# Kernel optimization log

Measured on AMD Instinct MI355X. Metric: run time of the kernel, lower is better.

The kernel has to match this reference:

```python
import jax, jax.numpy as jnp
import numpy as np

THRESHOLD = 1.5
MIN_AREA = 3
B, H, W = 8, 1024, 1024


def _label_components(mask):
    """8-connectivity connected-component labeling by min-index propagation.
    mask: [B,H,W] bool. Returns int32 labels [B,H,W]; each component is labeled
    by the minimum global flat index of its pixels; background pixels = B*H*W.
    Labels are globally unique across the batch (matches sort_labels' per-batch
    unique relabeling up to a label permutation).
    """
    N = B * H * W
    SENT = jnp.int32(N)
    flat = jnp.arange(N, dtype=jnp.int32).reshape(B, H, W)
    lab0 = jnp.where(mask, flat, SENT)

    def neighbor_min(lab):
        p = jnp.pad(lab, ((0, 0), (1, 1), (1, 1)), constant_values=N)
        m = lab
        for dr in (-1, 0, 1):
            for dc in (-1, 0, 1):
                if dr == 0 and dc == 0:
                    continue
                m = jnp.minimum(m, p[:, 1 + dr:1 + dr + H, 1 + dc:1 + dc + W])
        return jnp.where(mask, m, SENT)

    def cond(state):
        return state[1]

    def body(state):
        lab, _ = state
        new = neighbor_min(lab)
        return new, jnp.any(new != lab)

    lab, _ = jax.lax.while_loop(cond, body, (lab0, jnp.array(True)))
    return lab


def setup_inputs() -> dict:
    key = jax.random.key(0)
    x = jax.random.normal(key, (B, H, W // 1), dtype=jnp.float32)
    return {"input_tensor": x.reshape(B, 1, H, W)}


def reference(input_tensor):
    """Dense encoding of the original ragged output: for every pixel belonging
    to a cluster with area > MIN_AREA, emit the cluster's max value and the
    (row, col) of the first (lowest flat index) occurrence of that max;
    background / small-cluster pixels get (0, -1, -1). Since THRESHOLD > 0,
    max over masked_fill(0) in the original equals max over cluster pixels.
    """
    x = input_tensor[:, 0]                  # [B,H,W]
    N = B * H * W
    nseg = N + 1                            # last segment = background
    mask = (x >= THRESHOLD)
    ids = _label_components(mask).reshape(-1)          # [N] int32 in [0, N]
    vals = x.reshape(-1)
    fg = mask.reshape(-1)

    area = jax.ops.segment_sum(fg.astype(jnp.float32), ids, num_segments=nseg)
    cmax = jax.ops.segment_max(vals, ids, num_segments=nseg)

    within = jnp.tile(jnp.arange(H * W, dtype=jnp.int32), B)  # flat idx in image
    is_max = (vals == cmax[ids]) & fg
    cand = jnp.where(is_max, within, jnp.int32(H * W))
    amin = jax.ops.segment_min(cand, ids, num_segments=nseg)  # first argmax

    valid = fg & (area[ids] > MIN_AREA)
    out_max = jnp.where(valid, cmax[ids], jnp.float32(0.0)).reshape(B, H, W)
    aidx = amin[ids]
    row = jnp.where(valid, aidx // W, jnp.int32(-1)).reshape(B, H, W)
    col = jnp.where(valid, aidx % W, jnp.int32(-1)).reshape(B, H, W)
    return out_max, row, col
```

## Files before the change

### kernel.cpp

```cpp
#include <hip/hip_runtime.h>
#include <stdint.h>

#define THRESH 1.5f
constexpr int NPIX = 8 * 1024 * 1024;
constexpr int HW   = 1024 * 1024;
constexpr int WW   = 1024;
constexpr int NWORD = NPIX / 32;
constexpr int WPR   = WW / 32;

constexpr int BLK     = 256;
constexpr int GRD_PX4 = NPIX / (BLK * 4);
constexpr int GRD_W   = NWORD / BLK;

constexpr int SPB        = 640;
constexpr int BASE_SLOTS = GRD_W * SPB;
constexpr int OVF_SLOTS  = 16384;
constexpr int CAP        = BASE_SLOTS + OVF_SLOTS;

constexpr int WLSTRIDE = 1024;

__device__ __forceinline__ int find_root(const int* __restrict__ P, int x) {
    int p = P[x];
    while (p != x && p < NPIX) { x = p; p = P[x]; }
    return x;
}

__device__ __forceinline__ void merge(int* P, int a, int b) {
    int ra = find_root(P, a);
    int rb = find_root(P, b);
    while (ra != rb) {
        if (ra < rb) { int t = ra; ra = rb; rb = t; }
        int old = atomicCAS(&P[ra], ra, rb);
        if (old == ra) break;
        ra = find_root(P, old);
        rb = find_root(P, rb);
    }
}

__global__ void mask_init_k(const float* __restrict__ x, int* __restrict__ parent,
                            unsigned* __restrict__ mask, uint2* __restrict__ wl,
                            int* __restrict__ wl_cnt, int* __restrict__ ovf) {
    __shared__ unsigned s_nib[BLK];
    __shared__ int s_rank;
    int t  = threadIdx.x;
    int gt = blockIdx.x * BLK + t;
    int i4 = gt * 4;
    float4 v = *(const float4*)(x + i4);
    unsigned nib = (unsigned)(v.x >= THRESH) | ((unsigned)(v.y >= THRESH) << 1) |
                   ((unsigned)(v.z >= THRESH) << 2) | ((unsigned)(v.w >= THRESH) << 3);
    *(int4*)(parent + i4) = make_int4(i4, i4 + 1, i4 + 2, i4 + 3);
    if (t == 0) s_rank = 0;
    s_nib[t] = nib;
    __syncthreads();
    if ((t & 7) == 0) {
        unsigned w = 0;
        #pragma unroll
        for (int k = 0; k < 8; k++) w |= s_nib[t + k] << (4 * k);
        mask[gt >> 3] = w;
    }
    int nfg = __popc(nib);
    if (nfg) {
        int r = atomicAdd(&s_rank, nfg);
        uint2* dst = wl + (size_t)blockIdx.x * WLSTRIDE;
        if (nib & 1u) dst[r++] = make_uint2((unsigned)i4,     __float_as_uint(v.x));
        if (nib & 2u) dst[r++] = make_uint2((unsigned)i4 + 1, __float_as_uint(v.y));
        if (nib & 4u) dst[r++] = make_uint2((unsigned)i4 + 2, __float_as_uint(v.z));
        if (nib & 8u) dst[r++] = make_uint2((unsigned)i4 + 3, __float_as_uint(v.w));
    }
    __syncthreads();
    if (t == 0) wl_cnt[blockIdx.x] = s_rank;
    if (gt == 0) *ovf = 0;
}

__global__ void union_k(const unsigned* __restrict__ mask, int* __restrict__ parent) {
    int w = blockIdx.x * BLK + threadIdx.x;
    unsigned cur = mask[w];
    if (!cur) return;
    int r  = (w >> 5) & (WW - 1);
    int cw = w & (WPR - 1);
    unsigned prev = (cw > 0) ? mask[w - 1] : 0u;
    unsigned above = 0u, abovePrev = 0u, aboveNext = 0u;
    if (r > 0) {
        above     = mask[w - WPR];
        abovePrev = (cw > 0)       ? mask[w - WPR - 1] : 0u;
        aboveNext = (cw < WPR - 1) ? mask[w - WPR + 1] : 0u;
    }
    int base = w << 5;
    unsigned mW  = cur & ((cur   << 1) | (prev      >> 31));
    unsigned mN  = cur & above;
    unsigned mNW = cur & ((above << 1) | (abovePrev >> 31));
    unsigned mNE = cur & ((above >> 1) | ((aboveNext & 1u) << 31));
    while (mW)  { int b = __ffs(mW)  - 1; mW  &= mW  - 1; merge(parent, base + b, base + b - 1); }
    while (mN)  { int b = __ffs(mN)  - 1; mN  &= mN  - 1; merge(parent, base + b, base + b - WW); }
    while (mNW) { int b = __ffs(mNW) - 1; mNW &= mNW - 1; merge(parent, base + b, base + b - WW - 1); }
    while (mNE) { int b = __ffs(mNE) - 1; mNE &= mNE - 1; merge(parent, base + b, base + b - WW + 1); }
}

__global__ void claim_k(const unsigned* __restrict__ mask, int* __restrict__ parent,
                        int* __restrict__ cnt, unsigned long long* __restrict__ best,
                        int* __restrict__ ovf) {
    __shared__ int s_cnt;
    if (threadIdx.x == 0) s_cnt = 0;
    __syncthreads();
    int w = blockIdx.x * BLK + threadIdx.x;
    unsigned cur = mask[w];
    int base = w << 5;
    while (cur) {
        int b = __ffs(cur) - 1; cur &= cur - 1;
        int p = base + b;
        int root = find_root(parent, p);
        if (root == p) {
            int rank = atomicAdd(&s_cnt, 1);
            int slot;
            if (rank < SPB) slot = blockIdx.x * SPB + rank;
            else { int o = atomicAdd(ovf, 1); slot = BASE_SLOTS + (o < OVF_SLOTS ? o : OVF_SLOTS - 1); }
            cnt[slot] = 0; best[slot] = 0ull;
            parent[p] = NPIX + slot;
        } else {
            parent[p] = root;
        }
    }
}

__device__ __forceinline__ int compact_id(const int* __restrict__ P, int p) {
    int e = P[p];
    if (e < NPIX) e = P[e];
    return e - NPIX;
}

__global__ void stats_k(const uint2* __restrict__ wl, const int* __restrict__ wl_cnt,
                        const int* __restrict__ parent, int* __restrict__ cnt,
                        unsigned long long* __restrict__ best) {
    int region = blockIdx.x;
    int c = wl_cnt[region];
    const uint2* src = wl + (size_t)region * WLSTRIDE;
    for (int j = threadIdx.x; j < c; j += 64) {
        uint2 e = src[j];
        int p = (int)e.x;
        int cid = compact_id(parent, p);
        if (cid < 0 || cid >= CAP) continue;
        atomicAdd(&cnt[cid], 1);
        unsigned within = (unsigned)(p & (HW - 1));
        unsigned long long pk =
            ((unsigned long long)e.y << 32) | (unsigned long long)(~within);
        atomicMax(&best[cid], pk);
    }
}

__device__ __forceinline__ void lookup_one(const int* __restrict__ parent,
                                           const int* __restrict__ cnt,
                                           const unsigned long long* __restrict__ best,
                                           int p, float& om, float& orow, float& ocol) {
    int cid = compact_id(parent, p);
    if (cid >= 0 && cid < CAP && cnt[cid] > 3) {
        unsigned long long pk = best[cid];
        om   = __uint_as_float((unsigned)(pk >> 32));
        unsigned idx = ~((unsigned)pk);
        orow = (float)(idx >> 10);
        ocol = (float)(idx & (WW - 1));
    }
}

__global__ void out_k(const unsigned* __restrict__ mask, const int* __restrict__ parent,
                      const int* __restrict__ cnt,
                      const unsigned long long* __restrict__ best,
                      float* __restrict__ o) {
    int t = blockIdx.x * BLK + threadIdx.x;
    unsigned nib = (mask[t >> 3] >> ((t & 7) * 4)) & 0xFu;
    int i4 = t * 4;
    float4 m  = make_float4(0.f, 0.f, 0.f, 0.f);
    float4 rr = make_float4(-1.f, -1.f, -1.f, -1.f);
    float4 cc = make_float4(-1.f, -1.f, -1.f, -1.f);
    if (nib) {
        if (nib & 1u) lookup_one(parent, cnt, best, i4,     m.x, rr.x, cc.x);
        if (nib & 2u) lookup_one(parent, cnt, best, i4 + 1, m.y, rr.y, cc.y);
        if (nib & 4u) lookup_one(parent, cnt, best, i4 + 2, m.z, rr.z, cc.z);
        if (nib & 8u) lookup_one(parent, cnt, best, i4 + 3, m.w, rr.w, cc.w);
    }
    *(float4*)(o + i4)            = m;
    *(float4*)(o + NPIX + i4)     = rr;
    *(float4*)(o + 2 * NPIX + i4) = cc;
}

extern "C" void kernel_launch(void* const* d_in, const int* in_sizes, int n_in,
                              void* d_out, int out_size, void* d_ws, size_t ws_size,
                              hipStream_t stream) {
    const float* x = (const float*)d_in[0];
    float* o = (float*)d_out;

    char* base = (char*)d_ws;
    int* parent = (int*)base;
    size_t off = (size_t)NPIX * 4;
    unsigned long long* best = (unsigned long long*)(base + off);  off += (size_t)CAP * 8;
    int* cnt       = (int*)(base + off);                           off += (size_t)CAP * 4;
    unsigned* mask = (unsigned*)(base + off);                      off += (size_t)NWORD * 4;
    int* wl_cnt    = (int*)(base + off);                           off += (size_t)GRD_PX4 * 4;
    uint2* wl      = (uint2*)(base + off);                         off += (size_t)GRD_PX4 * WLSTRIDE * 8;
    int* ovf       = (int*)(base + off);

    mask_init_k<<<GRD_PX4, BLK, 0, stream>>>(x, parent, mask, wl, wl_cnt, ovf);
    union_k    <<<GRD_W,   BLK, 0, stream>>>(mask, parent);
    claim_k    <<<GRD_W,   BLK, 0, stream>>>(mask, parent, cnt, best, ovf);
    stats_k    <<<GRD_PX4, 64,  0, stream>>>(wl, wl_cnt, parent, cnt, best);
    out_k      <<<GRD_PX4, BLK, 0, stream>>>(mask, parent, cnt, best, o);
}
```

Before: 203.3 us.

## Fuse five CCL kernels into one cooperative kernel with grid syncs

Replaces the five separate launches (mask/init, union, claim, stats, output) with a single cooperative kernel of 1024 blocks that steps through the same phases, separated by grid-wide syncs. Phases 1 and 5 loop over several regions per block, and the stats phase assigns one wavefront per region. This is meant to remove launch gaps and per-kernel tail effects. In exchange it requires all blocks to be co-resident, limits occupancy to a fixed grid, and pays for grid.sync barriers.

```diff
diff --git a/kernel.cpp b/kernel.cpp
--- a/kernel.cpp
+++ b/kernel.cpp
@@ -1,19 +1,24 @@
 #include <hip/hip_runtime.h>
+#include <hip/hip_cooperative_groups.h>
 #include <stdint.h>
 
+namespace cg = cooperative_groups;
+
 #define THRESH 1.5f
-constexpr int NPIX = 8 * 1024 * 1024;
-constexpr int HW   = 1024 * 1024;
-constexpr int WW   = 1024;
+constexpr int NPIX  = 8 * 1024 * 1024;
+constexpr int HW    = 1024 * 1024;
+constexpr int WW    = 1024;
 constexpr int NWORD = NPIX / 32;
 constexpr int WPR   = WW / 32;
 
-constexpr int BLK     = 256;
-constexpr int GRD_PX4 = NPIX / (BLK * 4);
-constexpr int GRD_W   = NWORD / BLK;
+constexpr int BLK   = 256;
+constexpr int GRID  = 1024;
+constexpr int REGIONS  = NPIX / (BLK * 4);
+constexpr int P1_ITERS = REGIONS / GRID;
+static_assert(GRID * BLK == NWORD, "phase 2/3 assume exactly 1 word per thread");
 
 constexpr int SPB        = 640;
-constexpr int BASE_SLOTS = GRD_W * SPB;
+constexpr int BASE_SLOTS = GRID * SPB;
 constexpr int OVF_SLOTS  = 16384;
 constexpr int CAP        = BASE_SLOTS + OVF_SLOTS;
 
@@ -37,114 +42,10 @@
     }
 }
 
-__global__ void mask_init_k(const float* __restrict__ x, int* __restrict__ parent,
-                            unsigned* __restrict__ mask, uint2* __restrict__ wl,
-                            int* __restrict__ wl_cnt, int* __restrict__ ovf) {
-    __shared__ unsigned s_nib[BLK];
-    __shared__ int s_rank;
-    int t  = threadIdx.x;
-    int gt = blockIdx.x * BLK + t;
-    int i4 = gt * 4;
-    float4 v = *(const float4*)(x + i4);
-    unsigned nib = (unsigned)(v.x >= THRESH) | ((unsigned)(v.y >= THRESH) << 1) |
-                   ((unsigned)(v.z >= THRESH) << 2) | ((unsigned)(v.w >= THRESH) << 3);
-    *(int4*)(parent + i4) = make_int4(i4, i4 + 1, i4 + 2, i4 + 3);
-    if (t == 0) s_rank = 0;
-    s_nib[t] = nib;
-    __syncthreads();
-    if ((t & 7) == 0) {
-        unsigned w = 0;
-        #pragma unroll
-        for (int k = 0; k < 8; k++) w |= s_nib[t + k] << (4 * k);
-        mask[gt >> 3] = w;
-    }
-    int nfg = __popc(nib);
-    if (nfg) {
-        int r = atomicAdd(&s_rank, nfg);
-        uint2* dst = wl + (size_t)blockIdx.x * WLSTRIDE;
-        if (nib & 1u) dst[r++] = make_uint2((unsigned)i4,     __float_as_uint(v.x));
-        if (nib & 2u) dst[r++] = make_uint2((unsigned)i4 + 1, __float_as_uint(v.y));
-        if (nib & 4u) dst[r++] = make_uint2((unsigned)i4 + 2, __float_as_uint(v.z));
-        if (nib & 8u) dst[r++] = make_uint2((unsigned)i4 + 3, __float_as_uint(v.w));
-    }
-    __syncthreads();
-    if (t == 0) wl_cnt[blockIdx.x] = s_rank;
-    if (gt == 0) *ovf = 0;
-}
-
-__global__ void union_k(const unsigned* __restrict__ mask, int* __restrict__ parent) {
-    int w = blockIdx.x * BLK + threadIdx.x;
-    unsigned cur = mask[w];
-    if (!cur) return;
-    int r  = (w >> 5) & (WW - 1);
-    int cw = w & (WPR - 1);
-    unsigned prev = (cw > 0) ? mask[w - 1] : 0u;
-    unsigned above = 0u, abovePrev = 0u, aboveNext = 0u;
-    if (r > 0) {
-        above     = mask[w - WPR];
-        abovePrev = (cw > 0)       ? mask[w - WPR - 1] : 0u;
-        aboveNext = (cw < WPR - 1) ? mask[w - WPR + 1] : 0u;
-    }
-    int base = w << 5;
-    unsigned mW  = cur & ((cur   << 1) | (prev      >> 31));
-    unsigned mN  = cur & above;
-    unsigned mNW = cur & ((above << 1) | (abovePrev >> 31));
-    unsigned mNE = cur & ((above >> 1) | ((aboveNext & 1u) << 31));
-    while (mW)  { int b = __ffs(mW)  - 1; mW  &= mW  - 1; merge(parent, base + b, base + b - 1); }
-    while (mN)  { int b = __ffs(mN)  - 1; mN  &= mN  - 1; merge(parent, base + b, base + b - WW); }
-    while (mNW) { int b = __ffs(mNW) - 1; mNW &= mNW - 1; merge(parent, base + b, base + b - WW - 1); }
-    while (mNE) { int b = __ffs(mNE) - 1; mNE &= mNE - 1; merge(parent, base + b, base + b - WW + 1); }
-}
-
-__global__ void claim_k(const unsigned* __restrict__ mask, int* __restrict__ parent,
-                        int* __restrict__ cnt, unsigned long long* __restrict__ best,
-                        int* __restrict__ ovf) {
-    __shared__ int s_cnt;
-    if (threadIdx.x == 0) s_cnt = 0;
-    __syncthreads();
-    int w = blockIdx.x * BLK + threadIdx.x;
-    unsigned cur = mask[w];
-    int base = w << 5;
-    while (cur) {
-        int b = __ffs(cur) - 1; cur &= cur - 1;
-        int p = base + b;
-        int root = find_root(parent, p);
-        if (root == p) {
-            int rank = atomicAdd(&s_cnt, 1);
-            int slot;
-            if (rank < SPB) slot = blockIdx.x * SPB + rank;
-            else { int o = atomicAdd(ovf, 1); slot = BASE_SLOTS + (o < OVF_SLOTS ? o : OVF_SLOTS - 1); }
-            cnt[slot] = 0; best[slot] = 0ull;
-            parent[p] = NPIX + slot;
-        } else {
-            parent[p] = root;
-        }
-    }
-}
-
 __device__ __forceinline__ int compact_id(const int* __restrict__ P, int p) {
     int e = P[p];
     if (e < NPIX) e = P[e];
     return e - NPIX;
-}
-
-__global__ void stats_k(const uint2* __restrict__ wl, const int* __restrict__ wl_cnt,
-                        const int* __restrict__ parent, int* __restrict__ cnt,
-                        unsigned long long* __restrict__ best) {
-    int region = blockIdx.x;
-    int c = wl_cnt[region];
-    const uint2* src = wl + (size_t)region * WLSTRIDE;
-    for (int j = threadIdx.x; j < c; j += 64) {
-        uint2 e = src[j];
-        int p = (int)e.x;
-        int cid = compact_id(parent, p);
-        if (cid < 0 || cid >= CAP) continue;
-        atomicAdd(&cnt[cid], 1);
-        unsigned within = (unsigned)(p & (HW - 1));
-        unsigned long long pk =
-            ((unsigned long long)e.y << 32) | (unsigned long long)(~within);
-        atomicMax(&best[cid], pk);
-    }
 }
 
 __device__ __forceinline__ void lookup_one(const int* __restrict__ parent,
@@ -161,25 +62,140 @@
     }
 }
 
-__global__ void out_k(const unsigned* __restrict__ mask, const int* __restrict__ parent,
-                      const int* __restrict__ cnt,
-                      const unsigned long long* __restrict__ best,
-                      float* __restrict__ o) {
-    int t = blockIdx.x * BLK + threadIdx.x;
-    unsigned nib = (mask[t >> 3] >> ((t & 7) * 4)) & 0xFu;
-    int i4 = t * 4;
-    float4 m  = make_float4(0.f, 0.f, 0.f, 0.f);
-    float4 rr = make_float4(-1.f, -1.f, -1.f, -1.f);
-    float4 cc = make_float4(-1.f, -1.f, -1.f, -1.f);
-    if (nib) {
-        if (nib & 1u) lookup_one(parent, cnt, best, i4,     m.x, rr.x, cc.x);
-        if (nib & 2u) lookup_one(parent, cnt, best, i4 + 1, m.y, rr.y, cc.y);
-        if (nib & 4u) lookup_one(parent, cnt, best, i4 + 2, m.z, rr.z, cc.z);
-        if (nib & 8u) lookup_one(parent, cnt, best, i4 + 3, m.w, rr.w, cc.w);
-    }
-    *(float4*)(o + i4)            = m;
-    *(float4*)(o + NPIX + i4)     = rr;
-    *(float4*)(o + 2 * NPIX + i4) = cc;
+__global__ __launch_bounds__(BLK, 4) void fused_k(
+    const float* __restrict__ x, float* __restrict__ o,
+    int* __restrict__ parent, unsigned* __restrict__ mask,
+    uint2* __restrict__ wl, int* __restrict__ wl_cnt,
+    int* __restrict__ cnt, unsigned long long* __restrict__ best,
+    int* __restrict__ ovf)
+{
+    cg::grid_group grid = cg::this_grid();
+    __shared__ unsigned s_nib[BLK];
+    __shared__ int s_rank;
+    __shared__ int s_cnt;
+    const int t = threadIdx.x;
+
+    if (blockIdx.x == 0 && t == 0) *ovf = 0;
+
+    for (int it = 0; it < P1_ITERS; ++it) {
+        int v  = (int)blockIdx.x + it * GRID;
+        int gt = v * BLK + t;
+        int i4 = gt * 4;
+        float4 vx = *(const float4*)(x + i4);
+        unsigned nib = (unsigned)(vx.x >= THRESH) | ((unsigned)(vx.y >= THRESH) << 1) |
+                       ((unsigned)(vx.z >= THRESH) << 2) | ((unsigned)(vx.w >= THRESH) << 3);
+        *(int4*)(parent + i4) = make_int4(i4, i4 + 1, i4 + 2, i4 + 3);
+        if (t == 0) s_rank = 0;
+        s_nib[t] = nib;
+        __syncthreads();
+        if ((t & 7) == 0) {
+            unsigned w = 0;
+            #pragma unroll
+            for (int k = 0; k < 8; k++) w |= s_nib[t + k] << (4 * k);
+            mask[gt >> 3] = w;
+        }
+        int nfg = __popc(nib);
+        if (nfg) {
+            int r = atomicAdd(&s_rank, nfg);
+            uint2* dst = wl + (size_t)v * WLSTRIDE;
+            if (nib & 1u) dst[r++] = make_uint2((unsigned)i4,     __float_as_uint(vx.x));
+            if (nib & 2u) dst[r++] = make_uint2((unsigned)i4 + 1, __float_as_uint(vx.y));
+            if (nib & 4u) dst[r++] = make_uint2((unsigned)i4 + 2, __float_as_uint(vx.z));
+            if (nib & 8u) dst[r++] = make_uint2((unsigned)i4 + 3, __float_as_uint(vx.w));
+        }
+        __syncthreads();
+        if (t == 0) wl_cnt[v] = s_rank;
+    }
+    grid.sync();
+
+    {
+        int w = blockIdx.x * BLK + t;
+        unsigned cur = mask[w];
+        if (cur) {
+            int r  = (w >> 5) & (WW - 1);
+            int cw = w & (WPR - 1);
+            unsigned prev = (cw > 0) ? mask[w - 1] : 0u;
+            unsigned above = 0u, abovePrev = 0u, aboveNext = 0u;
+            if (r > 0) {
+                above     = mask[w - WPR];
+                abovePrev = (cw > 0)       ? mask[w - WPR - 1] : 0u;
+                aboveNext = (cw < WPR - 1) ? mask[w - WPR + 1] : 0u;
+            }
+            int base = w << 5;
+            unsigned mW  = cur & ((cur   << 1) | (prev      >> 31));
+            unsigned mN  = cur & above;
+            unsigned mNW = cur & ((above << 1) | (abovePrev >> 31));
+            unsigned mNE = cur & ((above >> 1) | ((aboveNext & 1u) << 31));
+            while (mW)  { int b = __ffs(mW)  - 1; mW  &= mW  - 1; merge(parent, base + b, base + b - 1); }
+            while (mN)  { int b = __ffs(mN)  - 1; mN  &= mN  - 1; merge(parent, base + b, base + b - WW); }
+            while (mNW) { int b = __ffs(mNW) - 1; mNW &= mNW - 1; merge(parent, base + b, base + b - WW - 1); }
+            while (mNE) { int b = __ffs(mNE) - 1; mNE &= mNE - 1; merge(parent, base + b, base + b - WW + 1); }
+        }
+    }
+    grid.sync();
+
+    {
+        if (t == 0) s_cnt = 0;
+        __syncthreads();
+        int w = blockIdx.x * BLK + t;
+        unsigned cur = mask[w];
+        int base = w << 5;
+        while (cur) {
+            int b = __ffs(cur) - 1; cur &= cur - 1;
+            int p = base + b;
+            int root = find_root(parent, p);
+            if (root == p) {
+                int rank = atomicAdd(&s_cnt, 1);
+                int slot;
+                if (rank < SPB) slot = blockIdx.x * SPB + rank;
+                else { int ofo = atomicAdd(ovf, 1); slot = BASE_SLOTS + (ofo < OVF_SLOTS ? ofo : OVF_SLOTS - 1); }
+                cnt[slot] = 0; best[slot] = 0ull;
+                parent[p] = NPIX + slot;
+            } else {
+                parent[p] = root;
+            }
+        }
+    }
+    grid.sync();
+
+    {
+        int gw   = (int)blockIdx.x * (BLK / 64) + (t >> 6);
+        int lane = t & 63;
+        for (int r = gw; r < REGIONS; r += GRID * (BLK / 64)) {
+            int c = wl_cnt[r];
+            const uint2* src = wl + (size_t)r * WLSTRIDE;
+            for (int j = lane; j < c; j += 64) {
+                uint2 e = src[j];
+                int p = (int)e.x;
+                int cid = compact_id(parent, p);
+                if (cid < 0 || cid >= CAP) continue;
+                atomicAdd(&cnt[cid], 1);
+                unsigned within = (unsigned)(p & (HW - 1));
+                unsigned long long pk =
+                    ((unsigned long long)e.y << 32) | (unsigned long long)(~within);
+                atomicMax(&best[cid], pk);
+            }
+        }
+    }
+    grid.sync();
+
+    for (int it = 0; it < P1_ITERS; ++it) {
+        int tt = ((int)blockIdx.x + it * GRID) * BLK + t;
+        unsigned nib = (mask[tt >> 3] >> ((tt & 7) * 4)) & 0xFu;
+        int i4 = tt * 4;
+        float4 m  = make_float4(0.f, 0.f, 0.f, 0.f);
+        float4 rr = make_float4(-1.f, -1.f, -1.f, -1.f);
+        float4 cc = make_float4(-1.f, -1.f, -1.f, -1.f);
+        if (nib) {
+            if (nib & 1u) lookup_one(parent, cnt, best, i4,     m.x, rr.x, cc.x);
+            if (nib & 2u) lookup_one(parent, cnt, best, i4 + 1, m.y, rr.y, cc.y);
+            if (nib & 4u) lookup_one(parent, cnt, best, i4 + 2, m.z, rr.z, cc.z);
+            if (nib & 8u) lookup_one(parent, cnt, best, i4 + 3, m.w, rr.w, cc.w);
+        }
+        *(float4*)(o + i4)            = m;
+        *(float4*)(o + NPIX + i4)     = rr;
+        *(float4*)(o + 2 * NPIX + i4) = cc;
+    }
 }
 
 extern "C" void kernel_launch(void* const* d_in, const int* in_sizes, int n_in,
@@ -194,13 +210,13 @@
     unsigned long long* best = (unsigned long long*)(base + off);  off += (size_t)CAP * 8;
     int* cnt       = (int*)(base + off);                           off += (size_t)CAP * 4;
     unsigned* mask = (unsigned*)(base + off);                      off += (size_t)NWORD * 4;
-    int* wl_cnt    = (int*)(base + off);                           off += (size_t)GRD_PX4 * 4;
-    uint2* wl      = (uint2*)(base + off);                         off += (size_t)GRD_PX4 * WLSTRIDE * 8;
+    int* wl_cnt    = (int*)(base + off);                           off += (size_t)REGIONS * 4;
+    uint2* wl      = (uint2*)(base + off);                         off += (size_t)REGIONS * WLSTRIDE * 8;
     int* ovf       = (int*)(base + off);
 
-    mask_init_k<<<GRD_PX4, BLK, 0, stream>>>(x, parent, mask, wl, wl_cnt, ovf);
-    union_k    <<<GRD_W,   BLK, 0, stream>>>(mask, parent);
-    claim_k    <<<GRD_W,   BLK, 0, stream>>>(mask, parent, cnt, best, ovf);
-    stats_k    <<<GRD_PX4, 64,  0, stream>>>(wl, wl_cnt, parent, cnt, best);
-    out_k      <<<GRD_PX4, BLK, 0, stream>>>(mask, parent, cnt, best, o);
-}
+    void* args[] = { (void*)&x, (void*)&o, (void*)&parent, (void*)&mask,
+                     (void*)&wl, (void*)&wl_cnt, (void*)&cnt, (void*)&best,
+                     (void*)&ovf };
+    hipLaunchCooperativeKernel((const void*)fused_k, dim3(GRID), dim3(BLK),
+                               args, 0, stream);
+}
```

Result: slower. 702.0 us (+245.2%).

## Fuse root claiming into stats kernel with lazy CAS-based compact ids

Applied to the files above, without the earlier changes.

Drops the separate claim kernel, which walked every mask word and path-compressed every pixel. Roots are now claimed lazily inside the stats pass: a global atomic counter hands out slots and a CAS marks each root, and each pixel's parent is overwritten with its compact id. The cnt and best tables are zeroed up front in mask_init, so the output lookup becomes a single parent read. The cost is contention on one global counter and racing CAS claims, with some slots wasted when a CAS loses, plus the extra zeroing writes.

```diff
diff --git a/kernel.cpp b/kernel.cpp
--- a/kernel.cpp
+++ b/kernel.cpp
@@ -2,9 +2,9 @@
 #include <stdint.h>
 
 #define THRESH 1.5f
-constexpr int NPIX = 8 * 1024 * 1024;
-constexpr int HW   = 1024 * 1024;
-constexpr int WW   = 1024;
+constexpr int NPIX  = 8 * 1024 * 1024;
+constexpr int HW    = 1024 * 1024;
+constexpr int WW    = 1024;
 constexpr int NWORD = NPIX / 32;
 constexpr int WPR   = WW / 32;
 
@@ -12,10 +12,9 @@
 constexpr int GRD_PX4 = NPIX / (BLK * 4);
 constexpr int GRD_W   = NWORD / BLK;
 
-constexpr int SPB        = 640;
-constexpr int BASE_SLOTS = GRD_W * SPB;
-constexpr int OVF_SLOTS  = 16384;
-constexpr int CAP        = BASE_SLOTS + OVF_SLOTS;
+constexpr int CAP = 671744;
+constexpr int ZINT4 = CAP * 12 / 16;
+static_assert((CAP * 12) % 16 == 0, "zero region must be int4-divisible");
 
 constexpr int WLSTRIDE = 1024;
 
@@ -39,11 +38,13 @@
 
 __global__ void mask_init_k(const float* __restrict__ x, int* __restrict__ parent,
                             unsigned* __restrict__ mask, uint2* __restrict__ wl,
-                            int* __restrict__ wl_cnt, int* __restrict__ ovf) {
+                            int* __restrict__ wl_cnt, int4* __restrict__ zbase,
+                            int* __restrict__ gcnt) {
     __shared__ unsigned s_nib[BLK];
     __shared__ int s_rank;
     int t  = threadIdx.x;
     int gt = blockIdx.x * BLK + t;
+    if (gt < ZINT4) zbase[gt] = make_int4(0, 0, 0, 0);
     int i4 = gt * 4;
     float4 v = *(const float4*)(x + i4);
     unsigned nib = (unsigned)(v.x >= THRESH) | ((unsigned)(v.y >= THRESH) << 1) |
@@ -69,7 +70,7 @@
     }
     __syncthreads();
     if (t == 0) wl_cnt[blockIdx.x] = s_rank;
-    if (gt == 0) *ovf = 0;
+    if (gt == 0) *gcnt = 0;
 }
 
 __global__ void union_k(const unsigned* __restrict__ mask, int* __restrict__ parent) {
@@ -96,49 +97,38 @@
     while (mNE) { int b = __ffs(mNE) - 1; mNE &= mNE - 1; merge(parent, base + b, base + b - WW + 1); }
 }
 
-__global__ void claim_k(const unsigned* __restrict__ mask, int* __restrict__ parent,
-                        int* __restrict__ cnt, unsigned long long* __restrict__ best,
-                        int* __restrict__ ovf) {
-    __shared__ int s_cnt;
-    if (threadIdx.x == 0) s_cnt = 0;
-    __syncthreads();
-    int w = blockIdx.x * BLK + threadIdx.x;
-    unsigned cur = mask[w];
-    int base = w << 5;
-    while (cur) {
-        int b = __ffs(cur) - 1; cur &= cur - 1;
-        int p = base + b;
-        int root = find_root(parent, p);
-        if (root == p) {
-            int rank = atomicAdd(&s_cnt, 1);
-            int slot;
-            if (rank < SPB) slot = blockIdx.x * SPB + rank;
-            else { int o = atomicAdd(ovf, 1); slot = BASE_SLOTS + (o < OVF_SLOTS ? o : OVF_SLOTS - 1); }
-            cnt[slot] = 0; best[slot] = 0ull;
-            parent[p] = NPIX + slot;
+__device__ __forceinline__ int claim_cid(int* __restrict__ P, int p,
+                                         int* __restrict__ gcnt) {
+    int x = p;
+    while (true) {
+        int e = P[x];
+        if (e >= NPIX) return e - NPIX;
+        if (e == x) {
+            int slot = atomicAdd(gcnt, 1);
+            if (slot >= CAP) slot = CAP - 1;
+            int old = atomicCAS(&P[x], x, NPIX + slot);
+            if (old == x)     return slot;
+            if (old >= NPIX)  return old - NPIX;
+            x = old;
         } else {
-            parent[p] = root;
+            x = e;
         }
     }
 }
 
-__device__ __forceinline__ int compact_id(const int* __restrict__ P, int p) {
-    int e = P[p];
-    if (e < NPIX) e = P[e];
-    return e - NPIX;
-}
-
-__global__ void stats_k(const uint2* __restrict__ wl, const int* __restrict__ wl_cnt,
-                        const int* __restrict__ parent, int* __restrict__ cnt,
-                        unsigned long long* __restrict__ best) {
+__global__ void cstats_k(const uint2* __restrict__ wl, const int* __restrict__ wl_cnt,
+                         int* __restrict__ parent, int* __restrict__ cnt,
+                         unsigned long long* __restrict__ best,
+                         int* __restrict__ gcnt) {
     int region = blockIdx.x;
     int c = wl_cnt[region];
     const uint2* src = wl + (size_t)region * WLSTRIDE;
     for (int j = threadIdx.x; j < c; j += 64) {
         uint2 e = src[j];
         int p = (int)e.x;
-        int cid = compact_id(parent, p);
+        int cid = claim_cid(parent, p, gcnt);
         if (cid < 0 || cid >= CAP) continue;
+        parent[p] = NPIX + cid;
         atomicAdd(&cnt[cid], 1);
         unsigned within = (unsigned)(p & (HW - 1));
         unsigned long long pk =
@@ -151,7 +141,7 @@
                                            const int* __restrict__ cnt,
                                            const unsigned long long* __restrict__ best,
                                            int p, float& om, float& orow, float& ocol) {
-    int cid = compact_id(parent, p);
+    int cid = parent[p] - NPIX;
     if (cid >= 0 && cid < CAP && cnt[cid] > 3) {
         unsigned long long pk = best[cid];
         om   = __uint_as_float((unsigned)(pk >> 32));
@@ -191,16 +181,16 @@
     char* base = (char*)d_ws;
     int* parent = (int*)base;
     size_t off = (size_t)NPIX * 4;
-    unsigned long long* best = (unsigned long long*)(base + off);  off += (size_t)CAP * 8;
+    unsigned long long* best = (unsigned long long*)(base + off);
+    int4* zbase = (int4*)(base + off);                             off += (size_t)CAP * 8;
     int* cnt       = (int*)(base + off);                           off += (size_t)CAP * 4;
     unsigned* mask = (unsigned*)(base + off);                      off += (size_t)NWORD * 4;
     int* wl_cnt    = (int*)(base + off);                           off += (size_t)GRD_PX4 * 4;
     uint2* wl      = (uint2*)(base + off);                         off += (size_t)GRD_PX4 * WLSTRIDE * 8;
-    int* ovf       = (int*)(base + off);
+    int* gcnt      = (int*)(base + off);
 
-    mask_init_k<<<GRD_PX4, BLK, 0, stream>>>(x, parent, mask, wl, wl_cnt, ovf);
+    mask_init_k<<<GRD_PX4, BLK, 0, stream>>>(x, parent, mask, wl, wl_cnt, zbase, gcnt);
     union_k    <<<GRD_W,   BLK, 0, stream>>>(mask, parent);
-    claim_k    <<<GRD_W,   BLK, 0, stream>>>(mask, parent, cnt, best, ovf);
-    stats_k    <<<GRD_PX4, 64,  0, stream>>>(wl, wl_cnt, parent, cnt, best);
+    cstats_k   <<<GRD_PX4, 64,  0, stream>>>(wl, wl_cnt, parent, cnt, best, gcnt);
     out_k      <<<GRD_PX4, BLK, 0, stream>>>(mask, parent, cnt, best, o);
 }
```

After: 378.3 us. 1.86x slower.
